# Kernel tuning notes

Measured on AMD Instinct MI355X. Metric: run time of the kernel, lower is better.

## Reference

```python
import jax, jax.numpy as jnp
import numpy as np

N_NODES = 8192
N_EDGES = 262144
IN_DIM = 128
HID = 128
FLAT = N_NODES * HID  # 1048576


def gcn_conv(x, edge_index, W, b):
    """PyG-style GCNConv: add self-loops, symmetric deg^{-1/2} normalization,
    out[col] += norm * (x @ W)[row], plus bias."""
    N = x.shape[0]
    loop = jnp.arange(N)
    row = jnp.concatenate([edge_index[0], loop])  # source nodes
    col = jnp.concatenate([edge_index[1], loop])  # target nodes
    deg = jax.ops.segment_sum(jnp.ones_like(col, dtype=x.dtype), col, num_segments=N)
    dinv = jax.lax.rsqrt(jnp.maximum(deg, 1.0))  # deg >= 1 thanks to self-loops
    norm = dinv[row] * dinv[col]  # [E+N]
    h = x @ W  # [N, out]
    msg = h[row] * norm[:, None]  # gather
    out = jax.ops.segment_sum(msg, col, num_segments=N)  # scatter-add
    return out + b


def setup_inputs() -> dict:
    key = jax.random.key(0)
    ks = jax.random.split(key, 12)
    def lin(k, fan_in, shape):
        bound = 1.0 / np.sqrt(fan_in)
        return jax.random.uniform(k, shape, jnp.float32, -bound, bound)
    return {
        "x": jax.random.normal(ks[0], (N_NODES, IN_DIM), jnp.float32),
        "edge_index": jax.random.randint(ks[1], (2, N_EDGES), 0, N_NODES, jnp.int64 if jax.config.jax_enable_x64 else jnp.int32),
        "W1": lin(ks[2], IN_DIM, (IN_DIM, HID)),
        "b1": lin(ks[3], IN_DIM, (HID,)),
        "W2": lin(ks[4], HID, (HID, HID)),
        "b2": lin(ks[5], HID, (HID,)),
        "fc1_w": lin(ks[6], FLAT, (FLAT, HID)),
        "fc1_b": lin(ks[7], FLAT, (HID,)),
        "fc2_w": lin(ks[8], HID, (HID, HID)),
        "fc2_b": lin(ks[9], HID, (HID,)),
        "fc3_w": lin(ks[10], HID, (HID, 1)),
        "fc3_b": lin(ks[11], HID, (1,)),
    }


def reference(x, edge_index, W1, b1, W2, b2, fc1_w, fc1_b, fc2_w, fc2_b, fc3_w, fc3_b):
    e = jax.nn.relu(gcn_conv(x, edge_index, W1, b1))
    e = gcn_conv(e, edge_index, W2, b2)
    flat = e.reshape(-1)  # [N_NODES*HID]
    h = jax.nn.relu(flat @ fc1_w + fc1_b)
    h = jax.nn.relu(h @ fc2_w + fc2_b)
    q = h @ fc3_w + fc3_b  # [1]
    return q
```

## Files before the change

### kernel.cpp

```cpp
#include <hip/hip_runtime.h>

#define N_NODES 8192
#define N_EDGES 262144
#define DIM 128

__global__ void k_deg(const int* __restrict__ col, int* __restrict__ deg) {
    int e = blockIdx.x * blockDim.x + threadIdx.x;
    if (e < N_EDGES) atomicAdd(&deg[col[e]], 1);
}

__global__ void k_dinv(const int* __restrict__ deg, float* __restrict__ dinv) {
    int i = blockIdx.x * blockDim.x + threadIdx.x;
    if (i < N_NODES) dinv[i] = rsqrtf((float)deg[i] + 1.0f);
}

__global__ __launch_bounds__(1024) void k_scan(const int* __restrict__ deg,
                                               int* __restrict__ rowptr) {
    __shared__ int part[1024];
    int t = threadIdx.x;
    int base = t * 8;
    int v[8];
    int s = 0;
    #pragma unroll
    for (int i = 0; i < 8; ++i) { v[i] = s; s += deg[base + i]; }
    part[t] = s;
    __syncthreads();
    for (int off = 1; off < 1024; off <<= 1) {
        int x = (t >= off) ? part[t - off] : 0;
        __syncthreads();
        part[t] += x;
        __syncthreads();
    }
    int basesum = (t == 0) ? 0 : part[t - 1];
    #pragma unroll
    for (int i = 0; i < 8; ++i) rowptr[base + i] = basesum + v[i];
    if (t == 1023) rowptr[8192] = part[1023];
}

__global__ void k_fill(const int* __restrict__ rows, const int* __restrict__ cols,
                       const int* __restrict__ rowptr, int* __restrict__ cnt,
                       int* __restrict__ srcs) {
    int e = blockIdx.x * blockDim.x + threadIdx.x;
    if (e < N_EDGES) {
        int c = cols[e];
        int p = atomicAdd(&cnt[c], 1);
        srcs[rowptr[c] + p] = rows[e];
    }
}

__global__ __launch_bounds__(256) void k_gemm(const float* __restrict__ x,
                                              const float* __restrict__ W,
                                              const float* __restrict__ dinv,
                                              float* __restrict__ out) {
    __shared__ float4 Wl[128 * 32];
    int t = threadIdx.x;
    const float4* W4 = (const float4*)W;
    for (int i = t; i < 128 * 32; i += 256) Wl[i] = W4[i];
    __syncthreads();

    int q  = t & 31;
    int rg = t >> 5;
    int row0 = blockIdx.x * 32;
    for (int p = 0; p < 4; ++p) {
        int row = row0 + p * 8 + rg;
        const float4* xr = (const float4*)(x + (size_t)row * DIM);
        float4 acc = {0.f, 0.f, 0.f, 0.f};
        #pragma unroll
        for (int k4 = 0; k4 < 32; ++k4) {
            float4 xv = xr[k4];
            float4 w0 = Wl[(k4 * 4 + 0) * 32 + q];
            float4 w1 = Wl[(k4 * 4 + 1) * 32 + q];
            float4 w2 = Wl[(k4 * 4 + 2) * 32 + q];
            float4 w3 = Wl[(k4 * 4 + 3) * 32 + q];
            acc.x += xv.x * w0.x + xv.y * w1.x + xv.z * w2.x + xv.w * w3.x;
            acc.y += xv.x * w0.y + xv.y * w1.y + xv.z * w2.y + xv.w * w3.y;
            acc.z += xv.x * w0.z + xv.y * w1.z + xv.z * w2.z + xv.w * w3.z;
            acc.w += xv.x * w0.w + xv.y * w1.w + xv.z * w2.w + xv.w * w3.w;
        }
        float s = dinv[row];
        acc.x *= s; acc.y *= s; acc.z *= s; acc.w *= s;
        ((float4*)(out + (size_t)row * DIM))[q] = acc;
    }
}

template <bool RELU>
__global__ __launch_bounds__(256) void k_gather(const float* __restrict__ h,
                                                const int* __restrict__ srcs,
                                                const int* __restrict__ rowptr,
                                                const float* __restrict__ dinv,
                                                const float* __restrict__ b,
                                                float* __restrict__ out) {
    int t = threadIdx.x;
    int lane = t & 63;
    int node = blockIdx.x * 4 + (t >> 6);
    const float2* H = (const float2*)h;
    int beg = rowptr[node];
    int end = rowptr[node + 1];
    float2 acc = H[(size_t)node * 64 + lane];
    int j = beg;
    for (; j + 1 < end; j += 2) {
        int r0 = srcs[j];
        int r1 = srcs[j + 1];
        float2 v0 = H[(size_t)r0 * 64 + lane];
        float2 v1 = H[(size_t)r1 * 64 + lane];
        acc.x += v0.x + v1.x;
        acc.y += v0.y + v1.y;
    }
    if (j < end) {
        int r = srcs[j];
        float2 v = H[(size_t)r * 64 + lane];
        acc.x += v.x;
        acc.y += v.y;
    }
    float s = dinv[node];
    float2 bv = ((const float2*)b)[lane];
    float2 o;
    o.x = s * acc.x + bv.x;
    o.y = s * acc.y + bv.y;
    if (RELU) { o.x = fmaxf(o.x, 0.f); o.y = fmaxf(o.y, 0.f); }
    ((float2*)(out + (size_t)node * DIM))[lane] = o;
}

__global__ __launch_bounds__(256) void k_fc1(const float* __restrict__ flat,
                                             const float* __restrict__ w,
                                             float* __restrict__ facc) {
    __shared__ float4 red[256];
    int t  = threadIdx.x;
    int q  = t & 31;
    int rg = t >> 5;
    int base = blockIdx.x * 512;
    float4 acc = {0.f, 0.f, 0.f, 0.f};
    for (int it = 0; it < 64; ++it) {
        int r = base + it * 8 + rg;
        float fv = flat[r];
        float4 wv = ((const float4*)(w + (size_t)r * DIM))[q];
        acc.x += fv * wv.x;
        acc.y += fv * wv.y;
        acc.z += fv * wv.z;
        acc.w += fv * wv.w;
    }
    red[t] = acc;
    __syncthreads();
    if (t < 32) {
        float4 s = red[t];
        for (int g = 1; g < 8; ++g) {
            float4 v = red[g * 32 + t];
            s.x += v.x; s.y += v.y; s.z += v.z; s.w += v.w;
        }
        float* dst = facc + t * 4;
        atomicAdd(dst + 0, s.x);
        atomicAdd(dst + 1, s.y);
        atomicAdd(dst + 2, s.z);
        atomicAdd(dst + 3, s.w);
    }
}

__global__ __launch_bounds__(128) void k_tail(const float* __restrict__ facc,
                                              const float* __restrict__ fc1_b,
                                              const float* __restrict__ fc2_w,
                                              const float* __restrict__ fc2_b,
                                              const float* __restrict__ fc3_w,
                                              const float* __restrict__ fc3_b,
                                              float* __restrict__ out) {
    __shared__ float h1[128], red[128];
    int j = threadIdx.x;
    h1[j] = fmaxf(facc[j] + fc1_b[j], 0.f);
    __syncthreads();
    float a = 0.f;
    #pragma unroll 8
    for (int k = 0; k < 128; ++k) a += h1[k] * fc2_w[k * 128 + j];
    float h2 = fmaxf(a + fc2_b[j], 0.f);
    red[j] = h2 * fc3_w[j];
    __syncthreads();
    if (j == 0) {
        float s = 0.f;
        for (int k = 0; k < 128; ++k) s += red[k];
        out[0] = s + fc3_b[0];
    }
}

extern "C" void kernel_launch(void* const* d_in, const int* in_sizes, int n_in,
                              void* d_out, int out_size, void* d_ws, size_t ws_size,
                              hipStream_t stream) {
    const float* x     = (const float*)d_in[0];
    const int*   ei    = (const int*)d_in[1];
    const float* W1    = (const float*)d_in[2];
    const float* b1    = (const float*)d_in[3];
    const float* W2    = (const float*)d_in[4];
    const float* b2    = (const float*)d_in[5];
    const float* fc1_w = (const float*)d_in[6];
    const float* fc1_b = (const float*)d_in[7];
    const float* fc2_w = (const float*)d_in[8];
    const float* fc2_b = (const float*)d_in[9];
    const float* fc3_w = (const float*)d_in[10];
    const float* fc3_b = (const float*)d_in[11];
    const int* rows = ei;
    const int* cols = ei + N_EDGES;

    float* buf0   = (float*)d_ws;
    float* buf1   = buf0 + (size_t)N_NODES * DIM;
    int*   degi   = (int*)(buf1 + (size_t)N_NODES * DIM);
    float* dinv   = (float*)(degi + N_NODES);
    int*   rowptr = (int*)(dinv + N_NODES);
    int*   cnt    = rowptr + N_NODES + 8;
    int*   srcs   = cnt + N_NODES;
    float* facc   = (float*)(srcs + N_EDGES);
    float* out    = (float*)d_out;

    hipMemsetAsync(degi, 0, N_NODES * sizeof(int), stream);
    hipMemsetAsync(cnt, 0, N_NODES * sizeof(int), stream);
    hipMemsetAsync(facc, 0, DIM * sizeof(float), stream);

    k_deg<<<N_EDGES / 256, 256, 0, stream>>>(cols, degi);
    k_dinv<<<N_NODES / 256, 256, 0, stream>>>(degi, dinv);
    k_scan<<<1, 1024, 0, stream>>>(degi, rowptr);
    k_fill<<<N_EDGES / 256, 256, 0, stream>>>(rows, cols, rowptr, cnt, srcs);

    k_gemm<<<N_NODES / 32, 256, 0, stream>>>(x, W1, dinv, buf0);
    k_gather<true><<<N_NODES / 4, 256, 0, stream>>>(buf0, srcs, rowptr, dinv, b1, buf1);

    k_gemm<<<N_NODES / 32, 256, 0, stream>>>(buf1, W2, dinv, buf0);
    k_gather<false><<<N_NODES / 4, 256, 0, stream>>>(buf0, srcs, rowptr, dinv, b2, buf1);

    k_fc1<<<2048, 256, 0, stream>>>(buf1, fc1_w, facc);
    k_tail<<<1, 128, 0, stream>>>(facc, fc1_b, fc2_w, fc2_b, fc3_w, fc3_b, out);
}
```

Before: 996.2 us.

## Fuse second GCN gather with fc1 matvec and merge dinv into scan

Fuses the second-layer neighbor aggregation with the fc1 matrix-vector product, so each block keeps its aggregated node rows in shared memory and streams its slice of fc1_w directly. The flattened embedding is no longer written and read back. The change also computes dinv inside the scan kernel, merges three memsets into one by reordering the workspace, and unrolls the gather loop by four. The cost is heavier per-block work in the fused kernel, and fc1 partial sums are now spread over 2048 blocks with atomics.

After: 873.5 us. -12.3%, faster.

```diff
diff --git a/kernel.cpp b/kernel.cpp
--- a/kernel.cpp
+++ b/kernel.cpp
@@ -9,20 +9,20 @@
     if (e < N_EDGES) atomicAdd(&deg[col[e]], 1);
 }
 
-__global__ void k_dinv(const int* __restrict__ deg, float* __restrict__ dinv) {
-    int i = blockIdx.x * blockDim.x + threadIdx.x;
-    if (i < N_NODES) dinv[i] = rsqrtf((float)deg[i] + 1.0f);
-}
-
 __global__ __launch_bounds__(1024) void k_scan(const int* __restrict__ deg,
-                                               int* __restrict__ rowptr) {
+                                               int* __restrict__ rowptr,
+                                               float* __restrict__ dinv) {
     __shared__ int part[1024];
     int t = threadIdx.x;
     int base = t * 8;
     int v[8];
     int s = 0;
     #pragma unroll
-    for (int i = 0; i < 8; ++i) { v[i] = s; s += deg[base + i]; }
+    for (int i = 0; i < 8; ++i) {
+        int d = deg[base + i];
+        dinv[base + i] = rsqrtf((float)d + 1.0f);
+        v[i] = s; s += d;
+    }
     part[t] = s;
     __syncthreads();
     for (int off = 1; off < 1024; off <<= 1) {
@@ -83,7 +83,6 @@
     }
 }
 
-template <bool RELU>
 __global__ __launch_bounds__(256) void k_gather(const float* __restrict__ h,
                                                 const int* __restrict__ srcs,
                                                 const int* __restrict__ rowptr,
@@ -98,60 +97,90 @@
     int end = rowptr[node + 1];
     float2 acc = H[(size_t)node * 64 + lane];
     int j = beg;
-    for (; j + 1 < end; j += 2) {
-        int r0 = srcs[j];
-        int r1 = srcs[j + 1];
+    for (; j + 3 < end; j += 4) {
+        int r0 = srcs[j], r1 = srcs[j + 1], r2 = srcs[j + 2], r3 = srcs[j + 3];
         float2 v0 = H[(size_t)r0 * 64 + lane];
         float2 v1 = H[(size_t)r1 * 64 + lane];
-        acc.x += v0.x + v1.x;
-        acc.y += v0.y + v1.y;
-    }
-    if (j < end) {
+        float2 v2 = H[(size_t)r2 * 64 + lane];
+        float2 v3 = H[(size_t)r3 * 64 + lane];
+        acc.x += (v0.x + v1.x) + (v2.x + v3.x);
+        acc.y += (v0.y + v1.y) + (v2.y + v3.y);
+    }
+    for (; j < end; ++j) {
         int r = srcs[j];
         float2 v = H[(size_t)r * 64 + lane];
-        acc.x += v.x;
-        acc.y += v.y;
+        acc.x += v.x; acc.y += v.y;
     }
     float s = dinv[node];
     float2 bv = ((const float2*)b)[lane];
     float2 o;
-    o.x = s * acc.x + bv.x;
-    o.y = s * acc.y + bv.y;
-    if (RELU) { o.x = fmaxf(o.x, 0.f); o.y = fmaxf(o.y, 0.f); }
+    o.x = fmaxf(s * acc.x + bv.x, 0.f);
+    o.y = fmaxf(s * acc.y + bv.y, 0.f);
     ((float2*)(out + (size_t)node * DIM))[lane] = o;
 }
 
-__global__ __launch_bounds__(256) void k_fc1(const float* __restrict__ flat,
+__global__ __launch_bounds__(256) void k_gfc(const float* __restrict__ h,
+                                             const int* __restrict__ srcs,
+                                             const int* __restrict__ rowptr,
+                                             const float* __restrict__ dinv,
+                                             const float* __restrict__ b,
                                              const float* __restrict__ w,
                                              float* __restrict__ facc) {
-    __shared__ float4 red[256];
-    int t  = threadIdx.x;
-    int q  = t & 31;
-    int rg = t >> 5;
-    int base = blockIdx.x * 512;
-    float4 acc = {0.f, 0.f, 0.f, 0.f};
-    for (int it = 0; it < 64; ++it) {
-        int r = base + it * 8 + rg;
-        float fv = flat[r];
-        float4 wv = ((const float4*)(w + (size_t)r * DIM))[q];
-        acc.x += fv * wv.x;
-        acc.y += fv * wv.y;
-        acc.z += fv * wv.z;
-        acc.w += fv * wv.w;
-    }
-    red[t] = acc;
-    __syncthreads();
-    if (t < 32) {
-        float4 s = red[t];
-        for (int g = 1; g < 8; ++g) {
-            float4 v = red[g * 32 + t];
-            s.x += v.x; s.y += v.y; s.z += v.z; s.w += v.w;
-        }
-        float* dst = facc + t * 4;
-        atomicAdd(dst + 0, s.x);
-        atomicAdd(dst + 1, s.y);
-        atomicAdd(dst + 2, s.z);
-        atomicAdd(dst + 3, s.w);
+    __shared__ float oL[4][128];
+    __shared__ float4 red4[4][32];
+    int t = threadIdx.x;
+    int lane = t & 63;
+    int wid = t >> 6;
+    int node = blockIdx.x * 4 + wid;
+    const float2* H = (const float2*)h;
+    int beg = rowptr[node];
+    int end = rowptr[node + 1];
+    float2 acc = H[(size_t)node * 64 + lane];
+    int j = beg;
+    for (; j + 3 < end; j += 4) {
+        int r0 = srcs[j], r1 = srcs[j + 1], r2 = srcs[j + 2], r3 = srcs[j + 3];
+        float2 v0 = H[(size_t)r0 * 64 + lane];
+        float2 v1 = H[(size_t)r1 * 64 + lane];
+        float2 v2 = H[(size_t)r2 * 64 + lane];
+        float2 v3 = H[(size_t)r3 * 64 + lane];
+        acc.x += (v0.x + v1.x) + (v2.x + v3.x);
+        acc.y += (v0.y + v1.y) + (v2.y + v3.y);
+    }
+    for (; j < end; ++j) {
+        int r = srcs[j];
+        float2 v = H[(size_t)r * 64 + lane];
+        acc.x += v.x; acc.y += v.y;
+    }
+    float s = dinv[node];
+    float2 bv = ((const float2*)b)[lane];
+    float2 o = { s * acc.x + bv.x, s * acc.y + bv.y };
+    ((float2*)oL[wid])[lane] = o;
+    __syncthreads();
+
+    int q  = lane & 31;
+    int kh = lane >> 5;
+    size_t rowbase = (size_t)node * 128;
+    float4 a4 = {0.f, 0.f, 0.f, 0.f};
+    #pragma unroll 8
+    for (int k2 = 0; k2 < 64; ++k2) {
+        int k = k2 * 2 + kh;
+        float ok = oL[wid][k];
+        float4 wr = ((const float4*)(w + (rowbase + k) * 128))[q];
+        a4.x += ok * wr.x;
+        a4.y += ok * wr.y;
+        a4.z += ok * wr.z;
+        a4.w += ok * wr.w;
+    }
+    a4.x += __shfl_xor(a4.x, 32);
+    a4.y += __shfl_xor(a4.y, 32);
+    a4.z += __shfl_xor(a4.z, 32);
+    a4.w += __shfl_xor(a4.w, 32);
+    if (lane < 32) red4[wid][q] = a4;
+    __syncthreads();
+    if (t < 128) {
+        const float* rf = (const float*)red4;
+        float val = (rf[t] + rf[128 + t]) + (rf[256 + t] + rf[384 + t]);
+        atomicAdd(&facc[t], val);
     }
 }
 
@@ -200,28 +229,24 @@
     float* buf0   = (float*)d_ws;
     float* buf1   = buf0 + (size_t)N_NODES * DIM;
     int*   degi   = (int*)(buf1 + (size_t)N_NODES * DIM);
-    float* dinv   = (float*)(degi + N_NODES);
+    int*   cnt    = degi + N_NODES;
+    float* facc   = (float*)(cnt + N_NODES);
+    float* dinv   = facc + DIM;
     int*   rowptr = (int*)(dinv + N_NODES);
-    int*   cnt    = rowptr + N_NODES + 8;
-    int*   srcs   = cnt + N_NODES;
-    float* facc   = (float*)(srcs + N_EDGES);
+    int*   srcs   = rowptr + N_NODES + 8;
     float* out    = (float*)d_out;
 
-    hipMemsetAsync(degi, 0, N_NODES * sizeof(int), stream);
-    hipMemsetAsync(cnt, 0, N_NODES * sizeof(int), stream);
-    hipMemsetAsync(facc, 0, DIM * sizeof(float), stream);
+    hipMemsetAsync(degi, 0, (2 * N_NODES) * sizeof(int) + DIM * sizeof(float), stream);
 
     k_deg<<<N_EDGES / 256, 256, 0, stream>>>(cols, degi);
-    k_dinv<<<N_NODES / 256, 256, 0, stream>>>(degi, dinv);
-    k_scan<<<1, 1024, 0, stream>>>(degi, rowptr);
+    k_scan<<<1, 1024, 0, stream>>>(degi, rowptr, dinv);
     k_fill<<<N_EDGES / 256, 256, 0, stream>>>(rows, cols, rowptr, cnt, srcs);
 
     k_gemm<<<N_NODES / 32, 256, 0, stream>>>(x, W1, dinv, buf0);
-    k_gather<true><<<N_NODES / 4, 256, 0, stream>>>(buf0, srcs, rowptr, dinv, b1, buf1);
+    k_gather<<<N_NODES / 4, 256, 0, stream>>>(buf0, srcs, rowptr, dinv, b1, buf1);
 
     k_gemm<<<N_NODES / 32, 256, 0, stream>>>(buf1, W2, dinv, buf0);
-    k_gather<false><<<N_NODES / 4, 256, 0, stream>>>(buf0, srcs, rowptr, dinv, b2, buf1);
-
-    k_fc1<<<2048, 256, 0, stream>>>(buf1, fc1_w, facc);
+    k_gfc<<<N_NODES / 4, 256, 0, stream>>>(buf0, srcs, rowptr, dinv, b2, fc1_w, facc);
+
     k_tail<<<1, 128, 0, stream>>>(facc, fc1_b, fc2_w, fc2_b, fc3_w, fc3_b, out);
 }
```
